# Kernel tuning notes

Measured on AMD Instinct MI355X. Metric: run time of the kernel, lower is better.

Reference implementation:

```python
import jax, jax.numpy as jnp
import numpy as np

REPEAT = 3
N, M, APM = 8192, 256, 32   # atoms, molecules, atoms per molecule
F_IN, D = 16, 64            # input atom features, hidden dim (d_e=d_v=d_u)


def _build_graph():
    k1 = np.arange(APM - 1)
    k2 = np.arange(APM - 2)
    pairs = np.concatenate([np.stack([k1, k1 + 1], 1), np.stack([k2, k2 + 2], 1)], 0)  # (61,2)
    base = (np.arange(M) * APM)[:, None, None]
    all_pairs = (pairs[None] + base).reshape(-1, 2)  # (E,2), upper triangular (left<right)
    return all_pairs[:, 0].astype(np.int32), all_pairs[:, 1].astype(np.int32)


def setup_inputs() -> dict:
    key = jax.random.key(0)
    ks = jax.random.split(key, 10)
    left, right = _build_graph()
    E = left.shape[0]  # 15616
    rng = np.random.default_rng(0)
    orders = rng.integers(1, 3, size=E).astype(np.float32)  # bond orders in {1,2}
    adj = np.zeros((N, N), np.float32)
    adj[left, right] = orders
    atom_in_mol = np.zeros((N, M), bool)
    atom_in_mol[np.arange(N), np.arange(N) // APM] = True
    bond_mol = left // APM
    bond_in_mol = np.zeros((E, M), bool)
    bond_in_mol[np.arange(E), bond_mol] = True

    def dense(k, fan_in, fan_out):
        return jax.random.normal(k, (fan_in, fan_out), jnp.float32) / np.sqrt(fan_in)

    return {
        'atoms': jax.random.normal(ks[0], (N, F_IN), jnp.float32),
        'adjacency_map': jnp.asarray(adj),
        'left_idxs': jnp.asarray(left),
        'right_idxs': jnp.asarray(right),
        'atom_in_mol': jnp.asarray(atom_in_mol),
        'bond_in_mol': jnp.asarray(bond_in_mol),
        'W_fe': dense(ks[1], 1, D), 'b_fe': jnp.zeros((D,), jnp.float32),
        'W_fv': dense(ks[2], F_IN, D), 'b_fv': jnp.zeros((D,), jnp.float32),
        'W_fu': dense(ks[3], F_IN, D), 'b_fu': jnp.zeros((D,), jnp.float32),
        'W_pe': dense(ks[4], 4 * D + 1, D), 'b_pe': jnp.zeros((D,), jnp.float32),
        'W_pv': dense(ks[5], 4 * D, D), 'b_pv': jnp.zeros((D,), jnp.float32),
        'W_pu': dense(ks[6], 4 * D, D), 'b_pu': jnp.zeros((D,), jnp.float32),
    }


def _graphnet(atoms, adjacency_map, left_idxs, right_idxs, atom_in_mol, bond_in_mol,
              W_fe, b_fe, W_fv, b_fv, W_fu, b_fu, W_pe, b_pe, W_pv, b_pv, W_pu, b_pu):
    n_atoms = atoms.shape[0]
    n_mols = atom_in_mol.shape[1]
    atom_mol = jnp.argmax(atom_in_mol, axis=1)   # (N,)  one mol per atom
    bond_mol = jnp.argmax(bond_in_mol, axis=1)   # (E,)  one mol per bond

    # f_e / f_v / f_u : initial edge, node, global embeddings
    bond_orders = adjacency_map[left_idxs, right_idxs]                  # (E,)
    h_e = jnp.tanh(bond_orders[:, None] @ W_fe + b_fe)                  # (E,D)
    h_v = jnp.tanh(atoms @ W_fv + b_fv)                                 # (N,D)
    atoms_per_mol = jax.ops.segment_sum(atoms, atom_mol, num_segments=n_mols)
    h_u = jnp.tanh(atoms_per_mol @ W_fu + b_fu)                         # (M,D)
    h_e0, h_v0, h_u0 = h_e, h_v, h_u

    for _ in range(REPEAT):
        # phi_e: per-edge update. TF's global term reduces over the feature
        # axis with keepdims -> a scalar per bond (faithful reproduction).
        h_left = h_v[left_idxs]
        h_right = h_v[right_idxs]
        u_e = jnp.sum(h_u[bond_mol], axis=1, keepdims=True)             # (E,1)
        h_e = jnp.tanh(jnp.concatenate([h_e, h_e0, h_left, h_right, u_e], -1) @ W_pe + b_pe)

        # rho_e_v: masked sum of edge features per incident atom == scatter-add
        h_e_bar_i = (jnp.zeros((n_atoms, h_e.shape[1]), h_e.dtype)
                     .at[left_idxs].add(h_e).at[right_idxs].add(h_e))   # (N,D)
        u_v = h_u[atom_mol]                                             # (N,D)
        h_v = jnp.tanh(jnp.concatenate([h_v, h_v0, h_e_bar_i, u_v], -1) @ W_pv + b_pv)

        # rho_e_u / rho_v_u: masked sums per molecule == segment sums
        h_e_bar = jax.ops.segment_sum(h_e, bond_mol, num_segments=n_mols)
        h_v_bar = jax.ops.segment_sum(h_v, atom_mol, num_segments=n_mols)
        h_u = jnp.tanh(jnp.concatenate([h_u, h_u0, h_e_bar, h_v_bar], -1) @ W_pu + b_pu)

    # default f_r = lambda *x: x[0] -> final edge representations
    return h_e


def reference(atoms, adjacency_map, left_idxs, right_idxs, atom_in_mol, bond_in_mol,
              W_fe, b_fe, W_fv, b_fv, W_fu, b_fu, W_pe, b_pe, W_pv, b_pv, W_pu, b_pu):
    return _graphnet(atoms, adjacency_map, left_idxs, right_idxs, atom_in_mol, bond_in_mol,
                     W_fe, b_fe, W_fv, b_fv, W_fu, b_fu, W_pe, b_pe, W_pv, b_pv, W_pu, b_pu)
```

## Files before the change

kernel.cpp:

```cpp
#include <hip/hip_runtime.h>

#define NATOMS 8192
#define NMOLS  256
#define APM    32
#define EPM    61
#define D      64
#define FIN    16
#define SE     72

typedef __bf16 bf16x8 __attribute__((ext_vector_type(8)));
typedef float  f32x4  __attribute__((ext_vector_type(4)));

#define MFMA_BF16(a, b, c) __builtin_amdgcn_mfma_f32_16x16x32_bf16((a), (b), (c), 0, 0, 0)

__device__ __forceinline__ ushort f2bf(float x) {
    uint u = __float_as_uint(x);
    u += 0x7fffu + ((u >> 16) & 1u);
    return (ushort)(u >> 16);
}
__device__ __forceinline__ float bf2f(ushort h) {
    return __uint_as_float(((uint)h) << 16);
}
__device__ __forceinline__ void split2(float x, ushort& h, ushort& l) {
    ushort hh = f2bf(x);
    h = hh;
    l = f2bf(x - bf2f(hh));
}
__device__ __forceinline__ float fast_tanh(float x) {
    float e = __builtin_amdgcn_exp2f(x * 2.885390081777926f);
    float r = __builtin_amdgcn_rcpf(e + 1.0f);
    return __builtin_fmaf(-2.0f, r, 1.0f);
}

union FragU { ushort u[8]; bf16x8 v; };

__device__ __forceinline__ void mfma3(const ushort* pH, const ushort* pL, int o,
                                      bf16x8 wH, bf16x8 wL,
                                      f32x4& accH, f32x4& accL) {
    bf16x8 ah = *(const bf16x8*)(pH + o);
    bf16x8 al = *(const bf16x8*)(pL + o);
    accH = MFMA_BF16(ah, wH, accH);
    accL = MFMA_BF16(al, wH, accL);
    accL = MFMA_BF16(ah, wL, accL);
}

__global__ __launch_bounds__(512, 2) void graphnet_kernel(
    const float* __restrict__ atoms,
    const float* __restrict__ adj,
    const int*   __restrict__ left,
    const int*   __restrict__ right,
    const float* __restrict__ Wfe, const float* __restrict__ bfe,
    const float* __restrict__ Wfv, const float* __restrict__ bfv,
    const float* __restrict__ Wfu, const float* __restrict__ bfu,
    const float* __restrict__ Wpe, const float* __restrict__ bpe,
    const float* __restrict__ Wpv, const float* __restrict__ bpv,
    const float* __restrict__ Wpu, const float* __restrict__ bpu,
    float* __restrict__ out)
{
    __shared__ __align__(16) ushort heH[2][64 * SE], heL[2][64 * SE];
    __shared__ __align__(16) ushort he0H[64 * SE], he0L[64 * SE];
    __shared__ __align__(16) ushort hvH[2][APM * SE], hvL[2][APM * SE];
    __shared__ __align__(16) ushort hv0H[APM * SE], hv0L[APM * SE];
    __shared__ __align__(16) ushort huH[D], huL[D];
    __shared__ float huF[D], hu0F[D];
    __shared__ float atoms_s[APM * FIN];
    __shared__ float apm_s[FIN];
    __shared__ float bo_s[EPM];
    __shared__ float parte[4][D];
    __shared__ float part2[2][D];
    __shared__ float hebar[D];
    __shared__ float phiu_part[8][D];
    __shared__ int   lloc[EPM], rloc[EPM];
    __shared__ int   inc[APM][4];

    const int tid  = threadIdx.x;
    const int lane = tid & 63;
    const int w    = tid >> 6;
    const int nt   = w & 3;
    const int mt2  = w >> 2;
    const int cb   = __builtin_amdgcn_readfirstlane(nt) * 16;
    const int lr   = lane & 15;
    const int kb   = lane >> 4;
    const int m    = blockIdx.x;

    if (tid < EPM) {
        int gl = left [m * EPM + tid];
        int gr = right[m * EPM + tid];
        lloc[tid] = gl - m * APM;
        rloc[tid] = gr - m * APM;
        bo_s[tid] = adj[(size_t)gl * NATOMS + gr];
    }
    if (tid < APM * FIN) atoms_s[tid] = atoms[(size_t)m * (APM * FIN) + tid];

    FragU feH[8], feL[8], fvH[8], fvL[8];
    #pragma unroll
    for (int s = 0; s < 8; ++s) {
        #pragma unroll
        for (int j = 0; j < 8; ++j) {
            split2(Wpe[(s * 32 + kb * 8 + j) * D + cb + lr], feH[s].u[j], feL[s].u[j]);
            split2(Wpv[(s * 32 + kb * 8 + j) * D + cb + lr], fvH[s].u[j], fvL[s].u[j]);
        }
    }
    float wpu_reg[32];
    #pragma unroll
    for (int kk = 0; kk < 32; ++kk)
        wpu_reg[kk] = Wpu[(w * 32 + kk) * D + lane];
    const float bias_e = bpe[cb + lr];
    const float w5_e   = Wpe[4 * D * D + cb + lr];
    const float bias_v = bpv[cb + lr];
    const float bpu_l  = bpu[lane];

    __syncthreads();

    if (tid < APM) {
        int dg = 0;
        for (int e = 0; e < EPM; ++e) {
            if (lloc[e] == tid) inc[tid][dg++] = e;
            if (rloc[e] == tid) inc[tid][dg++] = e;
        }
        for (int j = dg; j < 4; ++j) inc[tid][j] = 63;
    }
    if (tid < FIN) {
        float s = 0.f;
        for (int a = 0; a < APM; ++a) s += atoms_s[a * FIN + tid];
        apm_s[tid] = s;
    }
    #pragma unroll
    for (int i = 0; i < 4; ++i) {
        int idx = tid + 512 * i;
        int a = idx >> 6, c = idx & 63;
        float acc = bfv[c];
        #pragma unroll
        for (int f = 0; f < FIN; ++f) acc += atoms_s[a * FIN + f] * Wfv[f * D + c];
        float t = fast_tanh(acc);
        ushort h, l; split2(t, h, l);
        hvH[0][a * SE + c] = h; hvL[0][a * SE + c] = l;
        hv0H[a * SE + c] = h;   hv0L[a * SE + c] = l;
    }
    #pragma unroll
    for (int i = 0; i < 8; ++i) {
        int idx = tid + 512 * i;
        int e = idx >> 6, c = idx & 63;
        float t = 0.f;
        if (e < EPM) t = fast_tanh(bo_s[e] * Wfe[c] + bfe[c]);
        ushort h, l; split2(t, h, l);
        heH[0][e * SE + c] = h; heL[0][e * SE + c] = l;
        he0H[e * SE + c] = h;   he0L[e * SE + c] = l;
        if (e >= EPM) { heH[1][e * SE + c] = 0; heL[1][e * SE + c] = 0; }
    }
    __syncthreads();

    float hu_val;
    {
        float acc = bfu[lane];
        #pragma unroll
        for (int f = 0; f < FIN; ++f) acc += apm_s[f] * Wfu[f * D + lane];
        hu_val = fast_tanh(acc);
        if (w == 7) {
            huF[lane] = hu_val; hu0F[lane] = hu_val;
            split2(hu_val, huH[lane], huL[lane]);
        }
    }

    const int col  = cb + lr;
    const int e0   = mt2 * 16 + lr;
    const int e1   = e0 + 32;
    const int ec1  = (e1 < EPM) ? e1 : EPM - 1;
    const int la0  = lloc[e0],  ra0 = rloc[e0];
    const int la1  = lloc[ec1], ra1 = rloc[ec1];
    const int ofk  = kb * 8;
    const int arow = mt2 * 16 + lr;

    int cur = 0;
    for (int it = 0; it < 3; ++it) {
        const ushort* heHc = heH[cur]; const ushort* heLc = heL[cur];
        const ushort* hvHc = hvH[cur]; const ushort* hvLc = hvL[cur];

        f32x4 aH0 = {0,0,0,0}, aL0 = {0,0,0,0}, aH1 = {0,0,0,0}, aL1 = {0,0,0,0};
        mfma3(heHc + e0*SE,  heLc + e0*SE,  ofk,      feH[0].v, feL[0].v, aH0, aL0);
        mfma3(heHc + e1*SE,  heLc + e1*SE,  ofk,      feH[0].v, feL[0].v, aH1, aL1);
        mfma3(heHc + e0*SE,  heLc + e0*SE,  32 + ofk, feH[1].v, feL[1].v, aH0, aL0);
        mfma3(heHc + e1*SE,  heLc + e1*SE,  32 + ofk, feH[1].v, feL[1].v, aH1, aL1);
        mfma3(he0H + e0*SE,  he0L + e0*SE,  ofk,      feH[2].v, feL[2].v, aH0, aL0);
        mfma3(he0H + e1*SE,  he0L + e1*SE,  ofk,      feH[2].v, feL[2].v, aH1, aL1);
        mfma3(he0H + e0*SE,  he0L + e0*SE,  32 + ofk, feH[3].v, feL[3].v, aH0, aL0);
        mfma3(he0H + e1*SE,  he0L + e1*SE,  32 + ofk, feH[3].v, feL[3].v, aH1, aL1);
        mfma3(hvHc + la0*SE, hvLc + la0*SE, ofk,      feH[4].v, feL[4].v, aH0, aL0);
        mfma3(hvHc + la1*SE, hvLc + la1*SE, ofk,      feH[4].v, feL[4].v, aH1, aL1);
        mfma3(hvHc + la0*SE, hvLc + la0*SE, 32 + ofk, feH[5].v, feL[5].v, aH0, aL0);
        mfma3(hvHc + la1*SE, hvLc + la1*SE, 32 + ofk, feH[5].v, feL[5].v, aH1, aL1);
        mfma3(hvHc + ra0*SE, hvLc + ra0*SE, ofk,      feH[6].v, feL[6].v, aH0, aL0);
        mfma3(hvHc + ra1*SE, hvLc + ra1*SE, ofk,      feH[6].v, feL[6].v, aH1, aL1);
        mfma3(hvHc + ra0*SE, hvLc + ra0*SE, 32 + ofk, feH[7].v, feL[7].v, aH0, aL0);
        mfma3(hvHc + ra1*SE, hvLc + ra1*SE, 32 + ofk, feH[7].v, feL[7].v, aH1, aL1);

        if (it > 0) {
            float t = bpu_l;
            #pragma unroll
            for (int w8 = 0; w8 < 8; ++w8) t += phiu_part[w8][lane];
            hu_val = fast_tanh(t);
            if (w == 7) {
                huF[lane] = hu_val;
                split2(hu_val, huH[lane], huL[lane]);
            }
        }
        float uev = hu_val;
        #pragma unroll
        for (int off = 32; off; off >>= 1) uev += __shfl_xor(uev, off, 64);

        float out0[4], out1[4]; float ps0 = 0.f, ps1 = 0.f;
        #pragma unroll
        for (int r = 0; r < 4; ++r) {
            float t0 = fast_tanh(aH0[r] + aL0[r] + bias_e + uev * w5_e);
            float t1 = fast_tanh(aH1[r] + aL1[r] + bias_e + uev * w5_e);
            out0[r] = t0; out1[r] = t1;
            ps0 += t0;
            if (32 + mt2 * 16 + kb * 4 + r < EPM) ps1 += t1;
        }

        if (it == 2) {
            #pragma unroll
            for (int r = 0; r < 4; ++r) {
                int g0 = mt2 * 16 + kb * 4 + r;
                out[((size_t)(m * EPM + g0)) * D + col] = out0[r];
                int g1 = g0 + 32;
                if (g1 < EPM) out[((size_t)(m * EPM + g1)) * D + col] = out1[r];
            }
            return;
        }

        ps0 += __shfl_xor(ps0, 16, 64); ps0 += __shfl_xor(ps0, 32, 64);
        ps1 += __shfl_xor(ps1, 16, 64); ps1 += __shfl_xor(ps1, 32, 64);

        const int nxt = cur ^ 1;
        #pragma unroll
        for (int r = 0; r < 4; ++r) {
            int g0 = mt2 * 16 + kb * 4 + r;
            split2(out0[r], heH[nxt][g0 * SE + col], heL[nxt][g0 * SE + col]);
            int g1 = g0 + 32;
            if (g1 < EPM)
                split2(out1[r], heH[nxt][g1 * SE + col], heL[nxt][g1 * SE + col]);
        }
        if (kb == 0) { parte[mt2][col] = ps0; parte[2 + mt2][col] = ps1; }
        __syncthreads();

        if (tid < D)
            hebar[tid] = parte[0][tid] + parte[1][tid] + parte[2][tid] + parte[3][tid];

        const ushort* heHn = heH[nxt]; const ushort* heLn = heL[nxt];
        const int ie0 = inc[arow][0], ie1 = inc[arow][1];
        const int ie2 = inc[arow][2], ie3 = inc[arow][3];

        f32x4 vH = {0,0,0,0}, vL = {0,0,0,0};
        mfma3(hvHc + arow*SE, hvLc + arow*SE, ofk,      fvH[0].v, fvL[0].v, vH, vL);
        mfma3(hvHc + arow*SE, hvLc + arow*SE, 32 + ofk, fvH[1].v, fvL[1].v, vH, vL);
        mfma3(hv0H + arow*SE, hv0L + arow*SE, ofk,      fvH[2].v, fvL[2].v, vH, vL);
        mfma3(hv0H + arow*SE, hv0L + arow*SE, 32 + ofk, fvH[3].v, fvL[3].v, vH, vL);
        mfma3(heHn + ie0*SE, heLn + ie0*SE, ofk,      fvH[4].v, fvL[4].v, vH, vL);
        mfma3(heHn + ie0*SE, heLn + ie0*SE, 32 + ofk, fvH[5].v, fvL[5].v, vH, vL);
        mfma3(heHn + ie1*SE, heLn + ie1*SE, ofk,      fvH[4].v, fvL[4].v, vH, vL);
        mfma3(heHn + ie1*SE, heLn + ie1*SE, 32 + ofk, fvH[5].v, fvL[5].v, vH, vL);
        mfma3(heHn + ie2*SE, heLn + ie2*SE, ofk,      fvH[4].v, fvL[4].v, vH, vL);
        mfma3(heHn + ie2*SE, heLn + ie2*SE, 32 + ofk, fvH[5].v, fvL[5].v, vH, vL);
        mfma3(heHn + ie3*SE, heLn + ie3*SE, ofk,      fvH[4].v, fvL[4].v, vH, vL);
        mfma3(heHn + ie3*SE, heLn + ie3*SE, 32 + ofk, fvH[5].v, fvL[5].v, vH, vL);
        mfma3(huH, huL, ofk,      fvH[6].v, fvL[6].v, vH, vL);
        mfma3(huH, huL, 32 + ofk, fvH[7].v, fvL[7].v, vH, vL);

        float outv2[4]; float ps2 = 0.f;
        #pragma unroll
        for (int r = 0; r < 4; ++r) {
            float t = fast_tanh(vH[r] + vL[r] + bias_v);
            outv2[r] = t; ps2 += t;
        }
        ps2 += __shfl_xor(ps2, 16, 64); ps2 += __shfl_xor(ps2, 32, 64);
        #pragma unroll
        for (int r = 0; r < 4; ++r) {
            int g = mt2 * 16 + kb * 4 + r;
            split2(outv2[r], hvH[nxt][g * SE + col], hvL[nxt][g * SE + col]);
        }
        if (kb == 0) part2[mt2][col] = ps2;
        __syncthreads();

        {
            const int b  = w >> 1;
            const int k0 = (w & 1) * 32;
            float s = 0.f;
            #pragma unroll
            for (int kk = 0; kk < 32; ++kk) {
                int k = k0 + kk;
                float x = (b == 0) ? huF[k] : (b == 1) ? hu0F[k]
                        : (b == 2) ? hebar[k] : (part2[0][k] + part2[1][k]);
                s += x * wpu_reg[kk];
            }
            phiu_part[w][lane] = s;
        }
        __syncthreads();
        cur = nxt;
    }
}

extern "C" void kernel_launch(void* const* d_in, const int* in_sizes, int n_in,
                              void* d_out, int out_size, void* d_ws, size_t ws_size,
                              hipStream_t stream) {
    const float* atoms = (const float*)d_in[0];
    const float* adj   = (const float*)d_in[1];
    const int*   left  = (const int*)  d_in[2];
    const int*   right = (const int*)  d_in[3];
    const float* Wfe = (const float*)d_in[6];
    const float* bfe = (const float*)d_in[7];
    const float* Wfv = (const float*)d_in[8];
    const float* bfv = (const float*)d_in[9];
    const float* Wfu = (const float*)d_in[10];
    const float* bfu = (const float*)d_in[11];
    const float* Wpe = (const float*)d_in[12];
    const float* bpe = (const float*)d_in[13];
    const float* Wpv = (const float*)d_in[14];
    const float* bpv = (const float*)d_in[15];
    const float* Wpu = (const float*)d_in[16];
    const float* bpu = (const float*)d_in[17];

    graphnet_kernel<<<dim3(NMOLS), dim3(512), 0, stream>>>(
        atoms, adj, left, right,
        Wfe, bfe, Wfv, bfv, Wfu, bfu,
        Wpe, bpe, Wpv, bpv, Wpu, bpu,
        (float*)d_out);
}
```

Before: 42.22 us.

## Split MFMA accumulators and hoist next-iteration edge MFMAs before the global update

The low-order correction MFMAs now accumulate into two separate accumulators instead of one, which shortens the dependent MFMA chains. The edge-update MFMA block for the next iteration is issued right after the node update, ahead of the global phi_u reduction, and a sched_barrier keeps that order. The node MFMAs are also moved before the hebar reduction, and the incidence index loads are hoisted out of the loop. The aim is to overlap MFMA latency with the scalar reduction work, at the cost of more live accumulator registers under a 512-thread, 2-blocks-per-CU launch bound.

Measured after the change: 84.92 us. +101.1%, slower.

```diff
diff --git a/kernel.cpp b/kernel.cpp
--- a/kernel.cpp
+++ b/kernel.cpp
@@ -34,14 +34,14 @@
 
 union FragU { ushort u[8]; bf16x8 v; };
 
-__device__ __forceinline__ void mfma3(const ushort* pH, const ushort* pL, int o,
-                                      bf16x8 wH, bf16x8 wL,
-                                      f32x4& accH, f32x4& accL) {
+__device__ __forceinline__ void mfma3s(const ushort* pH, const ushort* pL, int o,
+                                       bf16x8 wH, bf16x8 wL,
+                                       f32x4& H, f32x4& La, f32x4& Lb) {
     bf16x8 ah = *(const bf16x8*)(pH + o);
     bf16x8 al = *(const bf16x8*)(pL + o);
-    accH = MFMA_BF16(ah, wH, accH);
-    accL = MFMA_BF16(al, wH, accL);
-    accL = MFMA_BF16(ah, wL, accL);
+    H  = MFMA_BF16(ah, wH, H);
+    La = MFMA_BF16(al, wH, La);
+    Lb = MFMA_BF16(ah, wL, Lb);
 }
 
 __global__ __launch_bounds__(512, 2) void graphnet_kernel(
@@ -170,29 +170,36 @@
     const int la1  = lloc[ec1], ra1 = rloc[ec1];
     const int ofk  = kb * 8;
     const int arow = mt2 * 16 + lr;
+    const int ie0 = inc[arow][0], ie1 = inc[arow][1];
+    const int ie2 = inc[arow][2], ie3 = inc[arow][3];
+
+    f32x4 aH0, aL0a, aL0b, aH1, aL1a, aL1b;
+
+#define PHIE_ISSUE(HC, LC, VHC, VLC)                                                       \
+    aH0 = (f32x4){0,0,0,0}; aL0a = (f32x4){0,0,0,0}; aL0b = (f32x4){0,0,0,0};              \
+    aH1 = (f32x4){0,0,0,0}; aL1a = (f32x4){0,0,0,0}; aL1b = (f32x4){0,0,0,0};              \
+    mfma3s((HC) + e0*SE,  (LC) + e0*SE,  ofk,      feH[0].v, feL[0].v, aH0, aL0a, aL0b);   \
+    mfma3s((HC) + e1*SE,  (LC) + e1*SE,  ofk,      feH[0].v, feL[0].v, aH1, aL1a, aL1b);   \
+    mfma3s((HC) + e0*SE,  (LC) + e0*SE,  32 + ofk, feH[1].v, feL[1].v, aH0, aL0a, aL0b);   \
+    mfma3s((HC) + e1*SE,  (LC) + e1*SE,  32 + ofk, feH[1].v, feL[1].v, aH1, aL1a, aL1b);   \
+    mfma3s(he0H + e0*SE,  he0L + e0*SE,  ofk,      feH[2].v, feL[2].v, aH0, aL0a, aL0b);   \
+    mfma3s(he0H + e1*SE,  he0L + e1*SE,  ofk,      feH[2].v, feL[2].v, aH1, aL1a, aL1b);   \
+    mfma3s(he0H + e0*SE,  he0L + e0*SE,  32 + ofk, feH[3].v, feL[3].v, aH0, aL0a, aL0b);   \
+    mfma3s(he0H + e1*SE,  he0L + e1*SE,  32 + ofk, feH[3].v, feL[3].v, aH1, aL1a, aL1b);   \
+    mfma3s((VHC) + la0*SE, (VLC) + la0*SE, ofk,      feH[4].v, feL[4].v, aH0, aL0a, aL0b); \
+    mfma3s((VHC) + la1*SE, (VLC) + la1*SE, ofk,      feH[4].v, feL[4].v, aH1, aL1a, aL1b); \
+    mfma3s((VHC) + la0*SE, (VLC) + la0*SE, 32 + ofk, feH[5].v, feL[5].v, aH0, aL0a, aL0b); \
+    mfma3s((VHC) + la1*SE, (VLC) + la1*SE, 32 + ofk, feH[5].v, feL[5].v, aH1, aL1a, aL1b); \
+    mfma3s((VHC) + ra0*SE, (VLC) + ra0*SE, ofk,      feH[6].v, feL[6].v, aH0, aL0a, aL0b); \
+    mfma3s((VHC) + ra1*SE, (VLC) + ra1*SE, ofk,      feH[6].v, feL[6].v, aH1, aL1a, aL1b); \
+    mfma3s((VHC) + ra0*SE, (VLC) + ra0*SE, 32 + ofk, feH[7].v, feL[7].v, aH0, aL0a, aL0b); \
+    mfma3s((VHC) + ra1*SE, (VLC) + ra1*SE, 32 + ofk, feH[7].v, feL[7].v, aH1, aL1a, aL1b);
 
     int cur = 0;
+    PHIE_ISSUE(heH[0], heL[0], hvH[0], hvL[0]);
+
     for (int it = 0; it < 3; ++it) {
-        const ushort* heHc = heH[cur]; const ushort* heLc = heL[cur];
-        const ushort* hvHc = hvH[cur]; const ushort* hvLc = hvL[cur];
-
-        f32x4 aH0 = {0,0,0,0}, aL0 = {0,0,0,0}, aH1 = {0,0,0,0}, aL1 = {0,0,0,0};
-        mfma3(heHc + e0*SE,  heLc + e0*SE,  ofk,      feH[0].v, feL[0].v, aH0, aL0);
-        mfma3(heHc + e1*SE,  heLc + e1*SE,  ofk,      feH[0].v, feL[0].v, aH1, aL1);
-        mfma3(heHc + e0*SE,  heLc + e0*SE,  32 + ofk, feH[1].v, feL[1].v, aH0, aL0);
-        mfma3(heHc + e1*SE,  heLc + e1*SE,  32 + ofk, feH[1].v, feL[1].v, aH1, aL1);
-        mfma3(he0H + e0*SE,  he0L + e0*SE,  ofk,      feH[2].v, feL[2].v, aH0, aL0);
-        mfma3(he0H + e1*SE,  he0L + e1*SE,  ofk,      feH[2].v, feL[2].v, aH1, aL1);
-        mfma3(he0H + e0*SE,  he0L + e0*SE,  32 + ofk, feH[3].v, feL[3].v, aH0, aL0);
-        mfma3(he0H + e1*SE,  he0L + e1*SE,  32 + ofk, feH[3].v, feL[3].v, aH1, aL1);
-        mfma3(hvHc + la0*SE, hvLc + la0*SE, ofk,      feH[4].v, feL[4].v, aH0, aL0);
-        mfma3(hvHc + la1*SE, hvLc + la1*SE, ofk,      feH[4].v, feL[4].v, aH1, aL1);
-        mfma3(hvHc + la0*SE, hvLc + la0*SE, 32 + ofk, feH[5].v, feL[5].v, aH0, aL0);
-        mfma3(hvHc + la1*SE, hvLc + la1*SE, 32 + ofk, feH[5].v, feL[5].v, aH1, aL1);
-        mfma3(hvHc + ra0*SE, hvLc + ra0*SE, ofk,      feH[6].v, feL[6].v, aH0, aL0);
-        mfma3(hvHc + ra1*SE, hvLc + ra1*SE, ofk,      feH[6].v, feL[6].v, aH1, aL1);
-        mfma3(hvHc + ra0*SE, hvLc + ra0*SE, 32 + ofk, feH[7].v, feL[7].v, aH0, aL0);
-        mfma3(hvHc + ra1*SE, hvLc + ra1*SE, 32 + ofk, feH[7].v, feL[7].v, aH1, aL1);
+        const int nxt = cur ^ 1;
 
         if (it > 0) {
             float t = bpu_l;
@@ -211,8 +218,8 @@
         float out0[4], out1[4]; float ps0 = 0.f, ps1 = 0.f;
         #pragma unroll
         for (int r = 0; r < 4; ++r) {
-            float t0 = fast_tanh(aH0[r] + aL0[r] + bias_e + uev * w5_e);
-            float t1 = fast_tanh(aH1[r] + aL1[r] + bias_e + uev * w5_e);
+            float t0 = fast_tanh(aH0[r] + aL0a[r] + aL0b[r] + bias_e + uev * w5_e);
+            float t1 = fast_tanh(aH1[r] + aL1a[r] + aL1b[r] + bias_e + uev * w5_e);
             out0[r] = t0; out1[r] = t1;
             ps0 += t0;
             if (32 + mt2 * 16 + kb * 4 + r < EPM) ps1 += t1;
@@ -232,7 +239,6 @@
         ps0 += __shfl_xor(ps0, 16, 64); ps0 += __shfl_xor(ps0, 32, 64);
         ps1 += __shfl_xor(ps1, 16, 64); ps1 += __shfl_xor(ps1, 32, 64);
 
-        const int nxt = cur ^ 1;
         #pragma unroll
         for (int r = 0; r < 4; ++r) {
             int g0 = mt2 * 16 + kb * 4 + r;
@@ -244,33 +250,32 @@
         if (kb == 0) { parte[mt2][col] = ps0; parte[2 + mt2][col] = ps1; }
         __syncthreads();
 
+        const ushort* hvHc = hvH[cur]; const ushort* hvLc = hvL[cur];
+        const ushort* heHn = heH[nxt]; const ushort* heLn = heL[nxt];
+
+        f32x4 vH = {0,0,0,0}, vLa = {0,0,0,0}, vLb = {0,0,0,0};
+        mfma3s(hvHc + arow*SE, hvLc + arow*SE, ofk,      fvH[0].v, fvL[0].v, vH, vLa, vLb);
+        mfma3s(hvHc + arow*SE, hvLc + arow*SE, 32 + ofk, fvH[1].v, fvL[1].v, vH, vLa, vLb);
+        mfma3s(hv0H + arow*SE, hv0L + arow*SE, ofk,      fvH[2].v, fvL[2].v, vH, vLa, vLb);
+        mfma3s(hv0H + arow*SE, hv0L + arow*SE, 32 + ofk, fvH[3].v, fvL[3].v, vH, vLa, vLb);
+        mfma3s(heHn + ie0*SE, heLn + ie0*SE, ofk,      fvH[4].v, fvL[4].v, vH, vLa, vLb);
+        mfma3s(heHn + ie0*SE, heLn + ie0*SE, 32 + ofk, fvH[5].v, fvL[5].v, vH, vLa, vLb);
+        mfma3s(heHn + ie1*SE, heLn + ie1*SE, ofk,      fvH[4].v, fvL[4].v, vH, vLa, vLb);
+        mfma3s(heHn + ie1*SE, heLn + ie1*SE, 32 + ofk, fvH[5].v, fvL[5].v, vH, vLa, vLb);
+        mfma3s(heHn + ie2*SE, heLn + ie2*SE, ofk,      fvH[4].v, fvL[4].v, vH, vLa, vLb);
+        mfma3s(heHn + ie2*SE, heLn + ie2*SE, 32 + ofk, fvH[5].v, fvL[5].v, vH, vLa, vLb);
+        mfma3s(heHn + ie3*SE, heLn + ie3*SE, ofk,      fvH[4].v, fvL[4].v, vH, vLa, vLb);
+        mfma3s(heHn + ie3*SE, heLn + ie3*SE, 32 + ofk, fvH[5].v, fvL[5].v, vH, vLa, vLb);
+        mfma3s(huH, huL, ofk,      fvH[6].v, fvL[6].v, vH, vLa, vLb);
+        mfma3s(huH, huL, 32 + ofk, fvH[7].v, fvL[7].v, vH, vLa, vLb);
+
         if (tid < D)
             hebar[tid] = parte[0][tid] + parte[1][tid] + parte[2][tid] + parte[3][tid];
 
-        const ushort* heHn = heH[nxt]; const ushort* heLn = heL[nxt];
-        const int ie0 = inc[arow][0], ie1 = inc[arow][1];
-        const int ie2 = inc[arow][2], ie3 = inc[arow][3];
-
-        f32x4 vH = {0,0,0,0}, vL = {0,0,0,0};
-        mfma3(hvHc + arow*SE, hvLc + arow*SE, ofk,      fvH[0].v, fvL[0].v, vH, vL);
-        mfma3(hvHc + arow*SE, hvLc + arow*SE, 32 + ofk, fvH[1].v, fvL[1].v, vH, vL);
-        mfma3(hv0H + arow*SE, hv0L + arow*SE, ofk,      fvH[2].v, fvL[2].v, vH, vL);
-        mfma3(hv0H + arow*SE, hv0L + arow*SE, 32 + ofk, fvH[3].v, fvL[3].v, vH, vL);
-        mfma3(heHn + ie0*SE, heLn + ie0*SE, ofk,      fvH[4].v, fvL[4].v, vH, vL);
-        mfma3(heHn + ie0*SE, heLn + ie0*SE, 32 + ofk, fvH[5].v, fvL[5].v, vH, vL);
-        mfma3(heHn + ie1*SE, heLn + ie1*SE, ofk,      fvH[4].v, fvL[4].v, vH, vL);
-        mfma3(heHn + ie1*SE, heLn + ie1*SE, 32 + ofk, fvH[5].v, fvL[5].v, vH, vL);
-        mfma3(heHn + ie2*SE, heLn + ie2*SE, ofk,      fvH[4].v, fvL[4].v, vH, vL);
-        mfma3(heHn + ie2*SE, heLn + ie2*SE, 32 + ofk, fvH[5].v, fvL[5].v, vH, vL);
-        mfma3(heHn + ie3*SE, heLn + ie3*SE, ofk,      fvH[4].v, fvL[4].v, vH, vL);
-        mfma3(heHn + ie3*SE, heLn + ie3*SE, 32 + ofk, fvH[5].v, fvL[5].v, vH, vL);
-        mfma3(huH, huL, ofk,      fvH[6].v, fvL[6].v, vH, vL);
-        mfma3(huH, huL, 32 + ofk, fvH[7].v, fvL[7].v, vH, vL);
-
         float outv2[4]; float ps2 = 0.f;
         #pragma unroll
         for (int r = 0; r < 4; ++r) {
-            float t = fast_tanh(vH[r] + vL[r] + bias_v);
+            float t = fast_tanh(vH[r] + vLa[r] + vLb[r] + bias_v);
             outv2[r] = t; ps2 += t;
         }
         ps2 += __shfl_xor(ps2, 16, 64); ps2 += __shfl_xor(ps2, 32, 64);
@@ -281,6 +286,9 @@
         }
         if (kb == 0) part2[mt2][col] = ps2;
         __syncthreads();
+
+        PHIE_ISSUE(heH[nxt], heL[nxt], hvH[nxt], hvL[nxt]);
+        __builtin_amdgcn_sched_barrier(0);
 
         {
             const int b  = w >> 1;
```
